# Kernel optimization log

Measured on AMD Instinct MI355X. Metric: run time of the kernel, lower is better.

The kernel has to match this reference:

```python
import jax, jax.numpy as jnp
import numpy as np

K_TOP = 4  # module's k; with k=4 all sorted elems are kept


def setup_inputs() -> dict:
    key = jax.random.key(0)
    k1, k2 = jax.random.split(key)
    x = jax.random.normal(k1, (16, 224, 224, 256), dtype=jnp.float32)
    pool_weights = jax.random.normal(k2, (1, 1, 1, 1, 4), dtype=jnp.float32) * 0.1
    return {"x": x, "pool_weights": pool_weights}


def reference(x, pool_weights):
    B, H, W, C = x.shape
    # 'same' padding: pad bottom/right if odd (no-op for even H, W)
    pad_b, pad_r = H % 2, W % 2
    if pad_b or pad_r:
        x = jnp.pad(x, ((0, 0), (0, pad_b), (0, pad_r), (0, 0)))
        H, W = H + pad_b, W + pad_r
    # Gather 2x2 windows: [B, H/2, W/2, C, 4]
    blocks = x.reshape(B, H // 2, 2, W // 2, 2, C)
    blocks = blocks.transpose(0, 1, 3, 5, 2, 4).reshape(B, H // 2, W // 2, C, 4)
    # Ascending sort of the 4 window elements (same result as the TF sort network)
    sorted_blocks = jnp.sort(blocks, axis=-1)
    # Keep top-k (largest k, still ascending) and softmax-weight them
    topk = sorted_blocks[..., 4 - K_TOP:]
    w = jax.nn.softmax(pool_weights, axis=-1)  # (1,1,1,1,k) broadcasts
    return jnp.sum(w * topk, axis=-1)  # [B, H/2, W/2, C]
```

## Files before the change

kernel.cpp:

```cpp
#include <hip/hip_runtime.h>


#define HW_IN   224
#define HW_OUT  112
#define C4      64
#define ROW4    (HW_IN * C4)

__device__ __forceinline__ void cswap(float& a, float& b) {
    float lo = fminf(a, b);
    float hi = fmaxf(a, b);
    a = lo; b = hi;
}

__device__ __forceinline__ float sort4_dot(float v0, float v1, float v2, float v3,
                                           float w0, float w1, float w2, float w3) {
    cswap(v0, v1);
    cswap(v2, v3);
    cswap(v0, v2);
    cswap(v1, v3);
    cswap(v1, v2);
    return fmaf(w0, v0, fmaf(w1, v1, fmaf(w2, v2, w3 * v3)));
}

__global__ __launch_bounds__(256) void SortPool2D_kernel(
    const float4* __restrict__ x,
    const float*  __restrict__ pw,
    float4*       __restrict__ out,
    int n4)
{
    int idx = blockIdx.x * blockDim.x + threadIdx.x;
    if (idx >= n4) return;

    float p0 = pw[0], p1 = pw[1], p2 = pw[2], p3 = pw[3];
    float m  = fmaxf(fmaxf(p0, p1), fmaxf(p2, p3));
    float e0 = expf(p0 - m), e1 = expf(p1 - m), e2 = expf(p2 - m), e3 = expf(p3 - m);
    float inv = 1.0f / (e0 + e1 + e2 + e3);
    e0 *= inv; e1 *= inv; e2 *= inv; e3 *= inv;

    int c  = idx & (C4 - 1);
    int t  = idx >> 6;
    int w  = t % HW_OUT;
    t      = t / HW_OUT;
    int h  = t % HW_OUT;
    int b  = t / HW_OUT;

    int base = ((b * HW_IN + 2 * h) * HW_IN + 2 * w) * C4 + c;

    float4 a00 = x[base];
    float4 a01 = x[base + C4];
    float4 a10 = x[base + ROW4];
    float4 a11 = x[base + ROW4 + C4];

    float4 r;
    r.x = sort4_dot(a00.x, a01.x, a10.x, a11.x, e0, e1, e2, e3);
    r.y = sort4_dot(a00.y, a01.y, a10.y, a11.y, e0, e1, e2, e3);
    r.z = sort4_dot(a00.z, a01.z, a10.z, a11.z, e0, e1, e2, e3);
    r.w = sort4_dot(a00.w, a01.w, a10.w, a11.w, e0, e1, e2, e3);

    out[idx] = r;
}

extern "C" void kernel_launch(void* const* d_in, const int* in_sizes, int n_in,
                              void* d_out, int out_size, void* d_ws, size_t ws_size,
                              hipStream_t stream) {
    const float4* x  = (const float4*)d_in[0];
    const float*  pw = (const float*)d_in[1];
    float4*       out = (float4*)d_out;

    int n4 = out_size / 4;
    int block = 256;
    int grid = (n4 + block - 1) / block;
    SortPool2D_kernel<<<grid, block, 0, stream>>>(x, pw, out, n4);
}
```

Before: 1.072 ms.

## Assign one output row per block and use nontemporal loads and stores

Each block now handles a whole output row (b,h) and loops 28 times over it, so the per-element div/mod index math and per-thread softmax setup are amortized across iterations. Loads and stores use nontemporal builtins so the streamed input and output bypass cache retention. This cuts the grid to 1792 blocks, which may lower memory-level parallelism if too few waves are resident on the device.

```diff
diff --git a/kernel.cpp b/kernel.cpp
--- a/kernel.cpp
+++ b/kernel.cpp
@@ -5,6 +5,10 @@
 #define HW_OUT  112
 #define C4      64
 #define ROW4    (HW_IN * C4)
+#define OROW4   (HW_OUT * C4)
+#define ITERS   (OROW4 / 256)
+
+typedef float f4 __attribute__((ext_vector_type(4)));
 
 __device__ __forceinline__ void cswap(float& a, float& b) {
     float lo = fminf(a, b);
@@ -23,13 +27,13 @@
 }
 
 __global__ __launch_bounds__(256) void SortPool2D_kernel(
-    const float4* __restrict__ x,
-    const float*  __restrict__ pw,
-    float4*       __restrict__ out,
-    int n4)
+    const f4* __restrict__ x,
+    const float* __restrict__ pw,
+    f4* __restrict__ out)
 {
-    int idx = blockIdx.x * blockDim.x + threadIdx.x;
-    if (idx >= n4) return;
+    int row = blockIdx.x;
+    int h   = row % HW_OUT;
+    int b   = row / HW_OUT;
 
     float p0 = pw[0], p1 = pw[1], p2 = pw[2], p3 = pw[3];
     float m  = fmaxf(fmaxf(p0, p1), fmaxf(p2, p3));
@@ -37,38 +41,40 @@
     float inv = 1.0f / (e0 + e1 + e2 + e3);
     e0 *= inv; e1 *= inv; e2 *= inv; e3 *= inv;
 
-    int c  = idx & (C4 - 1);
-    int t  = idx >> 6;
-    int w  = t % HW_OUT;
-    t      = t / HW_OUT;
-    int h  = t % HW_OUT;
-    int b  = t / HW_OUT;
+    int inBase  = (b * HW_IN + 2 * h) * ROW4;
+    int outBase = row * OROW4;
+    int t = threadIdx.x;
 
-    int base = ((b * HW_IN + 2 * h) * HW_IN + 2 * w) * C4 + c;
+#pragma unroll 2
+    for (int j = 0; j < ITERS; ++j) {
+        int i = j * 256 + t;
+        int c = i & (C4 - 1);
+        int w = i >> 6;
+        int o = inBase + (w << 7) + c;
 
-    float4 a00 = x[base];
-    float4 a01 = x[base + C4];
-    float4 a10 = x[base + ROW4];
-    float4 a11 = x[base + ROW4 + C4];
+        f4 a00 = __builtin_nontemporal_load(&x[o]);
+        f4 a01 = __builtin_nontemporal_load(&x[o + C4]);
+        f4 a10 = __builtin_nontemporal_load(&x[o + ROW4]);
+        f4 a11 = __builtin_nontemporal_load(&x[o + ROW4 + C4]);
 
-    float4 r;
-    r.x = sort4_dot(a00.x, a01.x, a10.x, a11.x, e0, e1, e2, e3);
-    r.y = sort4_dot(a00.y, a01.y, a10.y, a11.y, e0, e1, e2, e3);
-    r.z = sort4_dot(a00.z, a01.z, a10.z, a11.z, e0, e1, e2, e3);
-    r.w = sort4_dot(a00.w, a01.w, a10.w, a11.w, e0, e1, e2, e3);
+        f4 r;
+        r.x = sort4_dot(a00.x, a01.x, a10.x, a11.x, e0, e1, e2, e3);
+        r.y = sort4_dot(a00.y, a01.y, a10.y, a11.y, e0, e1, e2, e3);
+        r.z = sort4_dot(a00.z, a01.z, a10.z, a11.z, e0, e1, e2, e3);
+        r.w = sort4_dot(a00.w, a01.w, a10.w, a11.w, e0, e1, e2, e3);
 
-    out[idx] = r;
+        __builtin_nontemporal_store(r, &out[outBase + i]);
+    }
 }
 
 extern "C" void kernel_launch(void* const* d_in, const int* in_sizes, int n_in,
                               void* d_out, int out_size, void* d_ws, size_t ws_size,
                               hipStream_t stream) {
-    const float4* x  = (const float4*)d_in[0];
-    const float*  pw = (const float*)d_in[1];
-    float4*       out = (float4*)d_out;
+    const f4*    x   = (const f4*)d_in[0];
+    const float* pw  = (const float*)d_in[1];
+    f4*          out = (f4*)d_out;
 
-    int n4 = out_size / 4;
+    int grid  = 16 * HW_OUT;
     int block = 256;
-    int grid = (n4 + block - 1) / block;
-    SortPool2D_kernel<<<grid, block, 0, stream>>>(x, pw, out, n4);
+    SortPool2D_kernel<<<grid, block, 0, stream>>>(x, pw, out);
 }
```

After: 1.068 ms. No clear change (-0.3%).
